# Kernel tuning notes

Measured on AMD Instinct MI355X. Metric: run time of the kernel, lower is better.

## Reference

```python
import jax, jax.numpy as jnp
import numpy as np

DN = ('NCHW', 'OIHW', 'NCHW')

def conv(x, w, b=None, stride=(1, 1), pad=((0, 0), (0, 0))):
    y = jax.lax.conv_general_dilated(x, w, stride, pad, dimension_numbers=DN)
    return y if b is None else y + b[None, :, None, None]

def conv_t(x, w, b, stride, pad):
    # PyTorch ConvTranspose2d: weight (in, out, kH, kW), output (H-1)*s - 2p + k
    kH, kW = w.shape[2], w.shape[3]
    wt = jnp.flip(w, axis=(2, 3)).swapaxes(0, 1)  # -> (out, in, kH, kW)
    y = jax.lax.conv_general_dilated(
        x, wt, (1, 1),
        ((kH - 1 - pad[0], kH - 1 - pad[0]), (kW - 1 - pad[1], kW - 1 - pad[1])),
        lhs_dilation=stride, dimension_numbers=DN)
    return y + b[None, :, None, None]

def res_stack(x, rw1, rw2):
    # Residual: x + conv1x1(relu(conv3x3(relu(x)))), then final relu
    for i in range(rw1.shape[0]):
        h = conv(jax.nn.relu(x), rw1[i], None, (1, 1), ((1, 1), (1, 1)))
        h = conv(jax.nn.relu(h), rw2[i], None, (1, 1), ((0, 0), (0, 0)))
        x = x + h
    return jax.nn.relu(x)

def setup_inputs() -> dict:
    key = jax.random.key(0)
    ks = jax.random.split(key, 24)
    def w(i, shape, s=0.05):
        return jax.random.normal(ks[i], shape, jnp.float32) * s
    K, D = 512, 64
    inp = {
        'x': jax.random.normal(ks[0], (32, 2, 400, 600), jnp.float32),
        'enc_w1': w(1, (64, 2, 10, 11)), 'enc_b1': w(2, (64,)),
        'enc_w2': w(3, (128, 64, 12, 12), 0.02), 'enc_b2': w(4, (128,)),
        'enc_w3': w(5, (128, 128, 3, 3)), 'enc_b3': w(6, (128,)),
        'enc_res_w1': w(7, (2, 64, 128, 3, 3)), 'enc_res_w2': w(8, (2, 128, 64, 1, 1)),
        'pre_w': w(9, (64, 128, 1, 1)), 'pre_b': w(10, (64,)),
        'emb': jax.random.uniform(ks[11], (K, D), jnp.float32, -1.0 / K, 1.0 / K),
        'dec_w1': w(12, (128, 64, 3, 3)), 'dec_b1': w(13, (128,)),
        'dec_res_w1': w(14, (2, 64, 128, 3, 3)), 'dec_res_w2': w(15, (2, 128, 64, 1, 1)),
        'dec_tw1': w(16, (128, 64, 12, 12), 0.02), 'dec_tb1': w(17, (64,)),
        'dec_tw2': w(18, (64, 2, 10, 11)), 'dec_tb2': w(19, (2,)),
        'reset': 0,
    }
    return inp

def reference(x, enc_w1, enc_b1, enc_w2, enc_b2, enc_w3, enc_b3, enc_res_w1,
              enc_res_w2, pre_w, pre_b, emb, dec_w1, dec_b1, dec_res_w1,
              dec_res_w2, dec_tw1, dec_tb1, dec_tw2, dec_tb2, reset):
    commitment_cost = 0.25
    K = emb.shape[0]
    # Encoder
    h = jax.nn.relu(conv(x, enc_w1, enc_b1, (8, 9), ((1, 1), (1, 1))))
    h = jax.nn.relu(conv(h, enc_w2, enc_b2, (10, 10), ((1, 1), (1, 1))))
    h = conv(h, enc_w3, enc_b3, (1, 1), ((1, 1), (1, 1)))
    h = res_stack(h, enc_res_w1, enc_res_w2)
    z = conv(h, pre_w, pre_b)  # [B, D, H, W]
    # VectorQuantizer (eval mode)
    zin = z.transpose(0, 2, 3, 1)  # [B, H, W, D]
    B, H, W, D = zin.shape
    flat = zin.reshape(-1, D)
    dist = (jnp.sum(flat ** 2, axis=1, keepdims=True)
            + jnp.sum(emb ** 2, axis=1)
            - 2.0 * flat @ emb.T)  # [N, K]
    idx = jnp.argmin(dist, axis=1)  # [N]
    q = emb[idx].reshape(B, H, W, D)
    e_latent = jnp.mean((jax.lax.stop_gradient(q) - zin) ** 2)
    q_latent = jnp.mean((q - jax.lax.stop_gradient(zin)) ** 2)
    loss = q_latent + commitment_cost * e_latent
    q_st = zin + jax.lax.stop_gradient(q - zin)  # straight-through
    counts = jnp.zeros((K,), jnp.float32).at[idx].add(1.0)
    avg_probs = counts / flat.shape[0]
    perplexity = jnp.exp(-jnp.sum(avg_probs * jnp.log(avg_probs + 1e-10)))
    q_nchw = q_st.transpose(0, 3, 1, 2)
    # Decoder
    d = conv(q_nchw, dec_w1, dec_b1, (1, 1), ((1, 1), (1, 1)))
    d = res_stack(d, dec_res_w1, dec_res_w2)
    d = jax.nn.relu(conv_t(d, dec_tw1, dec_tb1, (10, 10), (1, 1)))
    recon = conv_t(d, dec_tw2, dec_tb2, (8, 9), (1, 1))
    return loss, recon, perplexity
```

## Files before the change

kernel.cpp:

```cpp
#include <hip/hip_runtime.h>
#include <math.h>


__global__ __launch_bounds__(256) void conv1_k(const float* __restrict__ x,
                                               const float* __restrict__ w,
                                               const float* __restrict__ b,
                                               float* __restrict__ y)
{
    __shared__ float xs[2 * 10 * 596];
    const int blk = blockIdx.x;
    const int n = blk / 50, oh = blk % 50;
    const int tid = threadIdx.x;
    const int ih0 = oh * 8 - 1;
    for (int i = tid; i < 2 * 10 * 596; i += 256) {
        int c = i / 5960, rem = i % 5960;
        int r = rem / 596, j = rem % 596;
        int ih = ih0 + r, iw = j - 1;
        float v = 0.f;
        if (ih >= 0 && ih < 400 && iw >= 0 && iw < 600)
            v = x[((n * 2 + c) * 400 + ih) * 600 + iw];
        xs[i] = v;
    }
    __syncthreads();
    for (int i = tid; i < 32 * 66; i += 256) {
        int oc = i / 66, ow = i % 66;
        int col = ow * 9;
        float a0 = 0.f, a1 = 0.f;
        for (int c = 0; c < 2; ++c) {
            const float* wp0 = w + ((oc)      * 2 + c) * 110;
            const float* wp1 = w + ((oc + 32) * 2 + c) * 110;
            const float* xp  = xs + c * 5960 + col;
            for (int kh = 0; kh < 10; ++kh) {
                #pragma unroll
                for (int kw = 0; kw < 11; ++kw) {
                    float xv = xp[kh * 596 + kw];
                    a0 += xv * wp0[kh * 11 + kw];
                    a1 += xv * wp1[kh * 11 + kw];
                }
            }
        }
        y[((n * 64 + oc)      * 50 + oh) * 66 + ow] = fmaxf(a0 + b[oc], 0.f);
        y[((n * 64 + oc + 32) * 50 + oh) * 66 + ow] = fmaxf(a1 + b[oc + 32], 0.f);
    }
}

__global__ __launch_bounds__(256) void repack_oihw_k(const float* __restrict__ w,
                                                     float* __restrict__ wt,
                                                     int OC, int IC, int KH, int KW)
{
    int i = blockIdx.x * 256 + threadIdx.x;
    int total = OC * IC * KH * KW;
    if (i >= total) return;
    int oc = i % OC; int t = i / OC;
    int kw = t % KW; int kh = (t / KW) % KH; int c = t / (KW * KH);
    wt[i] = w[((oc * IC + c) * KH + kh) * KW + kw];
}

__global__ __launch_bounds__(256) void repack_iohw_k(const float* __restrict__ w,
                                                     float* __restrict__ wt,
                                                     int IC, int OC, int KH, int KW)
{
    int i = blockIdx.x * 256 + threadIdx.x;
    int total = OC * IC * KH * KW;
    if (i >= total) return;
    int oc = i % OC; int t = i / OC;
    int kw = t % KW; int kh = (t / KW) % KH; int c = t / (KW * KH);
    wt[i] = w[((c * OC + oc) * KH + kh) * KW + kw];
}

__global__ __launch_bounds__(512) void conv2_k2(const float* __restrict__ x,
                                                const float* __restrict__ wt,
                                                const float* __restrict__ b,
                                                float* __restrict__ y)
{
    __shared__ float xs[16 * 12 * 64];
    __shared__ float sred[4 * 128 * 6];
    const int tid = threadIdx.x;
    const int oc = tid & 127, sub = tid >> 7;
    const int n = blockIdx.x / 5, oh = blockIdx.x % 5;
    const int ih0 = oh * 10 - 1;
    float acc[6] = {0, 0, 0, 0, 0, 0};
    for (int cc = 0; cc < 4; ++cc) {
        __syncthreads();
        for (int i = tid; i < 12288; i += 512) {
            int col = i & 63; int t2 = i >> 6;
            int r = t2 % 12; int c = t2 / 12;
            int ih = ih0 + r, iw = col - 1;
            float v = 0.f;
            if (ih >= 0 && ih < 50 && iw >= 0 && iw < 66)
                v = x[((n * 64 + cc * 16 + c) * 50 + ih) * 66 + iw];
            xs[i] = v;
        }
        __syncthreads();
        for (int c = 0; c < 16; ++c) {
            for (int kh = sub * 3; kh < sub * 3 + 3; ++kh) {
                float xr[64];
                #pragma unroll
                for (int k = 0; k < 16; ++k)
                    *(float4*)&xr[4 * k] = *(const float4*)&xs[(c * 12 + kh) * 64 + 4 * k];
                const float* wp = wt + ((cc * 16 + c) * 144 + kh * 12) * 128 + oc;
                #pragma unroll
                for (int kw = 0; kw < 12; ++kw) {
                    float wv = wp[kw * 128];
                    #pragma unroll
                    for (int ow = 0; ow < 6; ++ow)
                        acc[ow] += xr[ow * 10 + kw] * wv;
                }
            }
        }
    }
    for (int j = 0; j < 6; ++j) sred[(sub * 128 + oc) * 6 + j] = acc[j];
    __syncthreads();
    if (sub == 0) {
        float bias = b[oc];
        #pragma unroll
        for (int j = 0; j < 6; ++j) {
            float v = acc[j] + sred[(128 + oc) * 6 + j] + sred[(256 + oc) * 6 + j]
                    + sred[(384 + oc) * 6 + j] + bias;
            y[((n * 128 + oc) * 5 + oh) * 6 + j] = fmaxf(v, 0.f);
        }
    }
}

__global__ void conv3x3_k(const float* __restrict__ x, const float* __restrict__ w,
                          const float* __restrict__ b, float* __restrict__ y,
                          int Cin, int Cout, int relu_in)
{
    int idx = blockIdx.x * 256 + threadIdx.x;
    int total = 32 * Cout * 30;
    if (idx >= total) return;
    int ow = idx % 6, t = idx / 6;
    int oh = t % 5; t /= 5;
    int oc = t % Cout;
    int n = t / Cout;
    float acc = b ? b[oc] : 0.f;
    for (int kh = 0; kh < 3; ++kh) {
        int ih = oh - 1 + kh;
        if (ih < 0 || ih >= 5) continue;
        for (int kw = 0; kw < 3; ++kw) {
            int iw = ow - 1 + kw;
            if (iw < 0 || iw >= 6) continue;
            const float* xp = x + (n * Cin * 5 + ih) * 6 + iw;
            const float* wp = w + (oc * Cin * 3 + kh) * 3 + kw;
            #pragma unroll 4
            for (int c = 0; c < Cin; ++c) {
                float xv = xp[c * 30];
                if (relu_in) xv = fmaxf(xv, 0.f);
                acc += xv * wp[c * 9];
            }
        }
    }
    y[idx] = acc;
}

__global__ void res2_k(float* __restrict__ x, const float* __restrict__ t,
                       const float* __restrict__ w)
{
    int idx = blockIdx.x * 256 + threadIdx.x;
    if (idx >= 32 * 128 * 30) return;
    int ow = idx % 6;
    int oh = (idx / 6) % 5;
    int oc = (idx / 30) % 128;
    int n = idx / 3840;
    const float* tp = t + (n * 64 * 5 + oh) * 6 + ow;
    const float* wp = w + oc * 64;
    float acc = 0.f;
    #pragma unroll 4
    for (int c = 0; c < 64; ++c) acc += fmaxf(tp[c * 30], 0.f) * wp[c];
    x[idx] += acc;
}

__global__ void conv1x1_k(const float* __restrict__ x, const float* __restrict__ w,
                          const float* __restrict__ b, float* __restrict__ y)
{
    int idx = blockIdx.x * 256 + threadIdx.x;
    if (idx >= 32 * 64 * 30) return;
    int ow = idx % 6;
    int oh = (idx / 6) % 5;
    int oc = (idx / 30) % 64;
    int n = idx / 1920;
    const float* xp = x + (n * 128 * 5 + oh) * 6 + ow;
    const float* wp = w + oc * 128;
    float acc = b[oc];
    #pragma unroll 4
    for (int c = 0; c < 128; ++c) acc += fmaxf(xp[c * 30], 0.f) * wp[c];
    y[idx] = acc;
}

__global__ __launch_bounds__(64) void vq_k(const float* __restrict__ z,
                                           const float* __restrict__ emb,
                                           float* __restrict__ qn,
                                           float* __restrict__ counts,
                                           float* __restrict__ loss_sum)
{
    const int r = blockIdx.x;
    const int lane = threadIdx.x;
    const int n = r / 30, hw = r % 30;
    __shared__ float zs[64];
    zs[lane] = z[(n * 64 + lane) * 30 + hw];
    __syncthreads();
    float best = 1e30f;
    int bestk = 0;
    for (int j = 0; j < 8; ++j) {
        int k = lane + j * 64;
        const float* ep = emb + k * 64;
        float dist = 0.f;
        #pragma unroll 8
        for (int d = 0; d < 64; ++d) {
            float df = ep[d] - zs[d];
            dist += df * df;
        }
        if (dist < best) { best = dist; bestk = k; }
    }
    for (int off = 32; off > 0; off >>= 1) {
        float ob = __shfl_down(best, off);
        int ok = __shfl_down(bestk, off);
        if (ob < best || (ob == best && ok < bestk)) { best = ob; bestk = ok; }
    }
    bestk = __shfl(bestk, 0);
    float ev = emb[bestk * 64 + lane];
    qn[(n * 64 + lane) * 30 + hw] = ev;
    float df = ev - zs[lane];
    df *= df;
    for (int off = 32; off > 0; off >>= 1) df += __shfl_down(df, off);
    if (lane == 0) {
        atomicAdd(loss_sum, df);
        atomicAdd(&counts[bestk], 1.0f);
    }
}

__global__ __launch_bounds__(256) void xpad_k(const float* __restrict__ h,
                                              float* __restrict__ xp)
{
    int i = blockIdx.x * 256 + threadIdx.x;
    if (i >= 32 * 128 * 7 * 8) return;
    int col = i & 7; int t = i >> 3;
    int row = t % 7; t /= 7;
    int c = t % 128; int n = t / 128;
    float v = 0.f;
    if (row >= 1 && row <= 5 && col >= 1 && col <= 6)
        v = fmaxf(h[((n * 128 + c) * 5 + row - 1) * 6 + col - 1], 0.f);
    xp[i] = v;
}

__global__ __launch_bounds__(256) void convt1_k2(const float* __restrict__ xp,
                                                 const float* __restrict__ wt,
                                                 const float* __restrict__ b,
                                                 float* __restrict__ y)
{
    int gtid = blockIdx.x * 256 + threadIdx.x;
    int item = gtid >> 6;
    int lane = threadIdx.x & 63;
    int rw = item % 10; int t = item / 10;
    int rh = t % 10; t /= 10;
    int io = t % 5; int n = t / 5;
    int oh = 10 * io + (rh == 0 ? 9 : rh - 1);
    int kh0, i0, kh1 = 0, i1 = 0, nh = 1;
    if (rh == 0)      { kh0 = 0;  i0 = io + 1; kh1 = 10; i1 = io;     nh = 2; }
    else if (rh == 1) { kh0 = 1;  i0 = io;     kh1 = 11; i1 = io - 1; nh = 2; }
    else              { kh0 = rh; i0 = io; }
    int m0 = (rw == 0) ? 1 : 0;
    int kwa = rw, kwb = rw + 10;
    int nw = (rw < 2) ? 2 : 1;
    float acc[6] = {0, 0, 0, 0, 0, 0};
    for (int th = 0; th < nh; ++th) {
        int kh = th ? kh1 : kh0;
        int irow = th ? i1 : i0;
        const float* xr  = xp + ((n * 128) * 7 + irow + 1) * 8 + m0;
        const float* wpa = wt + (kh * 12 + kwa) * 64 + lane;
        const float* wpb = wt + (kh * 12 + kwb) * 64 + lane;
        for (int c = 0; c < 128; ++c) {
            float z[7];
            #pragma unroll
            for (int k = 0; k < 7; ++k) z[k] = xr[k];
            float wa = *wpa;
            #pragma unroll
            for (int j = 0; j < 6; ++j) acc[j] += z[j + 1] * wa;
            if (nw == 2) {
                float wb = *wpb;
                #pragma unroll
                for (int j = 0; j < 6; ++j) acc[j] += z[j] * wb;
            }
            xr += 56; wpa += 9216; wpb += 9216;
        }
    }
    float bias = b[lane];
    int colb = 10 * m0 + rw;
    float* yp = y + ((n * 64 + lane) * 52 + (oh + 1)) * 62 + colb;
    #pragma unroll
    for (int j = 0; j < 6; ++j) yp[10 * j] = fmaxf(acc[j] + bias, 0.f);
}

__global__ __launch_bounds__(256) void convt2_k2(const float* __restrict__ xd,
                                                 const float* __restrict__ wt2g,
                                                 const float* __restrict__ bb,
                                                 float* __restrict__ out)
{
    __shared__ __align__(16) float wl[14080];
    for (int i = threadIdx.x; i < 14080; i += 256) wl[i] = wt2g[i];
    __syncthreads();
    const int tid0 = blockIdx.x * 256 + threadIdx.x;
    const float b0 = bb[0], b1 = bb[1];
    for (int s = 0; s < 5; ++s) {
        int item = tid0 + s * 230400;
        int g = item % 10; int t = item / 10;
        int rw = t % 9; t /= 9;
        int rh = t % 8; t /= 8;
        int io = t % 50; int n = t / 50;
        int oh = 8 * io + (rh == 0 ? 7 : rh - 1);
        int kh0, i0, kh1 = 0, i1 = 0, nh = 1;
        if (rh == 0)      { kh0 = 0;  i0 = io + 1; kh1 = 8; i1 = io;     nh = 2; }
        else if (rh == 1) { kh0 = 1;  i0 = io;     kh1 = 9; i1 = io - 1; nh = 2; }
        else              { kh0 = rh; i0 = io; }
        int m0 = ((rw == 0) ? 1 : 0) + g * 6;
        int kwa = rw, kwb = rw + 9;
        int nw = (rw < 2) ? 2 : 1;
        float a0[6] = {0, 0, 0, 0, 0, 0}, a1[6] = {0, 0, 0, 0, 0, 0};
        for (int th = 0; th < nh; ++th) {
            int kh = th ? kh1 : kh0;
            int irow = th ? i1 : i0;
            const float* xr  = xd + ((n * 64) * 52 + irow + 1) * 62 + m0;
            const float* wpa = wl + (kh * 11 + kwa) * 2;
            const float* wpb = wl + (kh * 11 + kwb) * 2;
            for (int c = 0; c < 64; ++c) {
                float z[7];
                #pragma unroll
                for (int k = 0; k < 7; ++k) z[k] = xr[k];
                float2 wa = *(const float2*)wpa;
                #pragma unroll
                for (int j = 0; j < 6; ++j) { a0[j] += z[j + 1] * wa.x; a1[j] += z[j + 1] * wa.y; }
                if (nw == 2) {
                    float2 wb = *(const float2*)wpb;
                    #pragma unroll
                    for (int j = 0; j < 6; ++j) { a0[j] += z[j] * wb.x; a1[j] += z[j] * wb.y; }
                }
                xr += 3224; wpa += 220; wpb += 220;
            }
        }
        int colb = 9 * m0 + rw - 1;
        float* yp0 = out + ((n * 2 + 0) * 400 + oh) * 540 + colb;
        float* yp1 = out + ((n * 2 + 1) * 400 + oh) * 540 + colb;
        #pragma unroll
        for (int j = 0; j < 6; ++j) { yp0[9 * j] = a0[j] + b0; yp1[9 * j] = a1[j] + b1; }
    }
}

__global__ __launch_bounds__(512) void fin_k(const float* __restrict__ counts,
                                             const float* __restrict__ loss_sum,
                                             float* __restrict__ out, int out_size)
{
    __shared__ float red[512];
    int t = threadIdx.x;
    float c = counts[t];
    float p = c * (1.0f / 960.0f);
    red[t] = p * logf(p + 1e-10f);
    __syncthreads();
    for (int s = 256; s > 0; s >>= 1) {
        if (t < s) red[t] += red[t + s];
        __syncthreads();
    }
    if (t == 0) {
        out[out_size - 1] = expf(-red[0]);
        out[0] = loss_sum[0] * 1.25f / 61440.0f;
    }
}

extern "C" void kernel_launch(void* const* d_in, const int* in_sizes, int n_in,
                              void* d_out, int out_size, void* d_ws, size_t ws_size,
                              hipStream_t stream)
{
    const float* x          = (const float*)d_in[0];
    const float* enc_w1     = (const float*)d_in[1];
    const float* enc_b1     = (const float*)d_in[2];
    const float* enc_w2     = (const float*)d_in[3];
    const float* enc_b2     = (const float*)d_in[4];
    const float* enc_w3     = (const float*)d_in[5];
    const float* enc_b3     = (const float*)d_in[6];
    const float* enc_res_w1 = (const float*)d_in[7];
    const float* enc_res_w2 = (const float*)d_in[8];
    const float* pre_w      = (const float*)d_in[9];
    const float* pre_b      = (const float*)d_in[10];
    const float* emb        = (const float*)d_in[11];
    const float* dec_w1     = (const float*)d_in[12];
    const float* dec_b1     = (const float*)d_in[13];
    const float* dec_res_w1 = (const float*)d_in[14];
    const float* dec_res_w2 = (const float*)d_in[15];
    const float* dec_tw1    = (const float*)d_in[16];
    const float* dec_tb1    = (const float*)d_in[17];
    const float* dec_tw2    = (const float*)d_in[18];
    const float* dec_tb2    = (const float*)d_in[19];

    float* ws  = (float*)d_ws;
    float* out = (float*)d_out;

    float* h1       = ws;
    float* h2       = ws + 6758400;
    float* hA       = ws + 6881280;
    float* t64      = ws + 7004160;
    float* z        = ws + 7065600;
    float* qn       = ws + 7127040;
    float* counts   = ws + 7188480;
    float* loss_sum = ws + 7188992;
    float* wtA      = ws + 7189056;
    float* wt2      = ws + 8368704;
    float* xpad     = ws + 8382784;
    float* dmid     = ws;

    hipMemsetAsync(counts, 0, 513 * sizeof(float), stream);

    repack_oihw_k<<<4608, 256, 0, stream>>>(enc_w2, wtA, 128, 64, 12, 12);
    conv1_k<<<1600, 256, 0, stream>>>(x, enc_w1, enc_b1, h1);
    conv2_k2<<<160, 512, 0, stream>>>(h1, wtA, enc_b2, h2);
    conv3x3_k<<<480, 256, 0, stream>>>(h2, enc_w3, enc_b3, hA, 128, 128, 0);
    for (int i = 0; i < 2; ++i) {
        conv3x3_k<<<240, 256, 0, stream>>>(hA, enc_res_w1 + i * 73728, nullptr, t64, 128, 64, 1);
        res2_k<<<480, 256, 0, stream>>>(hA, t64, enc_res_w2 + i * 8192);
    }
    conv1x1_k<<<240, 256, 0, stream>>>(hA, pre_w, pre_b, z);

    repack_iohw_k<<<4608, 256, 0, stream>>>(dec_tw1, wtA, 128, 64, 12, 12);
    repack_iohw_k<<<55, 256, 0, stream>>>(dec_tw2, wt2, 64, 2, 10, 11);

    vq_k<<<960, 64, 0, stream>>>(z, emb, qn, counts, loss_sum);

    conv3x3_k<<<480, 256, 0, stream>>>(qn, dec_w1, dec_b1, h2, 64, 128, 0);
    for (int i = 0; i < 2; ++i) {
        conv3x3_k<<<240, 256, 0, stream>>>(h2, dec_res_w1 + i * 73728, nullptr, t64, 128, 64, 1);
        res2_k<<<480, 256, 0, stream>>>(h2, t64, dec_res_w2 + i * 8192);
    }
    xpad_k<<<896, 256, 0, stream>>>(h2, xpad);
    hipMemsetAsync(dmid, 0, (size_t)6601728 * sizeof(float), stream);
    convt1_k2<<<4000, 256, 0, stream>>>(xpad, wtA, dec_tb1, dmid);
    convt2_k2<<<900, 256, 0, stream>>>(dmid, wt2, dec_tb2, out + 1);

    fin_k<<<1, 512, 0, stream>>>(counts, loss_sum, out, out_size);
}
```

Baseline: 1.858 ms.

## Fuse latent-stage convs and VQ into one per-sample kernel; retile transposed convs

Replaces the chain of small latent-resolution kernels (enc conv3, residual stacks, pre-conv, VQ, decoder conv1, decoder residuals, padding) with a single 32-block kernel that keeps activations in LDS, using pre-repacked weights. Both transposed-conv kernels are rewritten so each block stages its input rows in LDS and reuses them across output phases. This removes many launches and global round-trips, but the fused kernel runs on only 32 blocks, which may leave most of the GPU idle.

```diff
diff --git a/kernel.cpp b/kernel.cpp
--- a/kernel.cpp
+++ b/kernel.cpp
@@ -66,6 +66,37 @@
     int oc = i % OC; int t = i / OC;
     int kw = t % KW; int kh = (t / KW) % KH; int c = t / (KW * KH);
     wt[i] = w[((c * OC + oc) * KH + kh) * KW + kw];
+}
+
+__device__ __forceinline__ float fetch_oihw(const float* __restrict__ w, int j,
+                                            int OC, int IC, int KH, int KW)
+{
+    int oc = j % OC; int t = j / OC;
+    int kw = t % KW; int kh = (t / KW) % KH; int c = t / (KW * KH);
+    return w[((oc * IC + c) * KH + kh) * KW + kw];
+}
+
+__global__ __launch_bounds__(256) void repack_small_k(
+    const float* __restrict__ enc_w3, const float* __restrict__ er1,
+    const float* __restrict__ er2, const float* __restrict__ pre_w,
+    const float* __restrict__ dec_w1, const float* __restrict__ dr1,
+    const float* __restrict__ dr2, float* __restrict__ dst)
+{
+    int i = blockIdx.x * 256 + threadIdx.x;
+    if (i >= 557056) return;
+    float v;
+    if (i < 147456)       v = fetch_oihw(enc_w3,        i,          128, 128, 3, 3);
+    else if (i < 221184)  v = fetch_oihw(er1,           i - 147456,  64, 128, 3, 3);
+    else if (i < 294912)  v = fetch_oihw(er1 + 73728,   i - 221184,  64, 128, 3, 3);
+    else if (i < 303104)  v = fetch_oihw(er2,           i - 294912, 128,  64, 1, 1);
+    else if (i < 311296)  v = fetch_oihw(er2 + 8192,    i - 303104, 128,  64, 1, 1);
+    else if (i < 319488)  v = fetch_oihw(pre_w,         i - 311296,  64, 128, 1, 1);
+    else if (i < 393216)  v = fetch_oihw(dec_w1,        i - 319488, 128,  64, 3, 3);
+    else if (i < 466944)  v = fetch_oihw(dr1,           i - 393216,  64, 128, 3, 3);
+    else if (i < 540672)  v = fetch_oihw(dr1 + 73728,   i - 466944,  64, 128, 3, 3);
+    else if (i < 548864)  v = fetch_oihw(dr2,           i - 540672, 128,  64, 1, 1);
+    else                  v = fetch_oihw(dr2 + 8192,    i - 548864, 128,  64, 1, 1);
+    dst[i] = v;
 }
 
 __global__ __launch_bounds__(512) void conv2_k2(const float* __restrict__ x,
@@ -122,226 +153,300 @@
     }
 }
 
-__global__ void conv3x3_k(const float* __restrict__ x, const float* __restrict__ w,
-                          const float* __restrict__ b, float* __restrict__ y,
-                          int Cin, int Cout, int relu_in)
-{
-    int idx = blockIdx.x * 256 + threadIdx.x;
-    int total = 32 * Cout * 30;
-    if (idx >= total) return;
-    int ow = idx % 6, t = idx / 6;
-    int oh = t % 5; t /= 5;
-    int oc = t % Cout;
-    int n = t / Cout;
-    float acc = b ? b[oc] : 0.f;
-    for (int kh = 0; kh < 3; ++kh) {
-        int ih = oh - 1 + kh;
-        if (ih < 0 || ih >= 5) continue;
-        for (int kw = 0; kw < 3; ++kw) {
-            int iw = ow - 1 + kw;
-            if (iw < 0 || iw >= 6) continue;
-            const float* xp = x + (n * Cin * 5 + ih) * 6 + iw;
-            const float* wp = w + (oc * Cin * 3 + kh) * 3 + kw;
-            #pragma unroll 4
-            for (int c = 0; c < Cin; ++c) {
-                float xv = xp[c * 30];
-                if (relu_in) xv = fmaxf(xv, 0.f);
-                acc += xv * wp[c * 9];
+
+template<int CIN, int COUT, bool RELU_IN>
+__device__ __forceinline__ void conv3x3_lds(const float* __restrict__ src,
+                                            const float* __restrict__ w,
+                                            const float* __restrict__ bias,
+                                            float* __restrict__ dst, int tid)
+{
+    constexpr int G = 512 / COUT;
+    const int oc = tid % COUT;
+    const int g  = tid / COUT;
+    const int px0 = (30 * g) / G;
+    const int np  = (30 * (g + 1)) / G - px0;
+    float bv = bias ? bias[oc] : 0.f;
+    float acc[8];
+    #pragma unroll
+    for (int j = 0; j < 8; ++j) acc[j] = bv;
+    for (int c = 0; c < CIN; ++c) {
+        const float* wc = w + c * 9 * COUT + oc;
+        const float* sc = src + c * 30;
+        #pragma unroll
+        for (int kh = 0; kh < 3; ++kh) {
+            #pragma unroll
+            for (int kw = 0; kw < 3; ++kw) {
+                float wv = wc[(kh * 3 + kw) * COUT];
+                #pragma unroll
+                for (int j = 0; j < 8; ++j) {
+                    if (j < np) {
+                        int px = px0 + j;
+                        int oh = px / 6, ow = px - oh * 6;
+                        int ih = oh + kh - 1, iw = ow + kw - 1;
+                        if ((unsigned)ih < 5u && (unsigned)iw < 6u) {
+                            float xv = sc[ih * 6 + iw];
+                            if (RELU_IN) xv = fmaxf(xv, 0.f);
+                            acc[j] += xv * wv;
+                        }
+                    }
+                }
             }
         }
     }
-    y[idx] = acc;
-}
-
-__global__ void res2_k(float* __restrict__ x, const float* __restrict__ t,
-                       const float* __restrict__ w)
-{
-    int idx = blockIdx.x * 256 + threadIdx.x;
-    if (idx >= 32 * 128 * 30) return;
-    int ow = idx % 6;
-    int oh = (idx / 6) % 5;
-    int oc = (idx / 30) % 128;
-    int n = idx / 3840;
-    const float* tp = t + (n * 64 * 5 + oh) * 6 + ow;
-    const float* wp = w + oc * 64;
-    float acc = 0.f;
-    #pragma unroll 4
-    for (int c = 0; c < 64; ++c) acc += fmaxf(tp[c * 30], 0.f) * wp[c];
-    x[idx] += acc;
-}
-
-__global__ void conv1x1_k(const float* __restrict__ x, const float* __restrict__ w,
-                          const float* __restrict__ b, float* __restrict__ y)
-{
-    int idx = blockIdx.x * 256 + threadIdx.x;
-    if (idx >= 32 * 64 * 30) return;
-    int ow = idx % 6;
-    int oh = (idx / 6) % 5;
-    int oc = (idx / 30) % 64;
-    int n = idx / 1920;
-    const float* xp = x + (n * 128 * 5 + oh) * 6 + ow;
-    const float* wp = w + oc * 128;
-    float acc = b[oc];
-    #pragma unroll 4
-    for (int c = 0; c < 128; ++c) acc += fmaxf(xp[c * 30], 0.f) * wp[c];
-    y[idx] = acc;
-}
-
-__global__ __launch_bounds__(64) void vq_k(const float* __restrict__ z,
-                                           const float* __restrict__ emb,
-                                           float* __restrict__ qn,
-                                           float* __restrict__ counts,
-                                           float* __restrict__ loss_sum)
-{
-    const int r = blockIdx.x;
-    const int lane = threadIdx.x;
-    const int n = r / 30, hw = r % 30;
-    __shared__ float zs[64];
-    zs[lane] = z[(n * 64 + lane) * 30 + hw];
-    __syncthreads();
-    float best = 1e30f;
-    int bestk = 0;
+    #pragma unroll
+    for (int j = 0; j < 8; ++j)
+        if (j < np) dst[oc * 30 + px0 + j] = acc[j];
+}
+
+template<int CIN, int COUT, bool RELU_IN, bool ACCUM>
+__device__ __forceinline__ void conv1x1_lds(const float* __restrict__ src,
+                                            const float* __restrict__ w,
+                                            const float* __restrict__ bias,
+                                            float* __restrict__ dst, int tid)
+{
+    constexpr int G = 512 / COUT;
+    const int oc = tid % COUT;
+    const int g  = tid / COUT;
+    const int px0 = (30 * g) / G;
+    const int np  = (30 * (g + 1)) / G - px0;
+    float bv = bias ? bias[oc] : 0.f;
+    float acc[8];
+    #pragma unroll
+    for (int j = 0; j < 8; ++j) acc[j] = bv;
+    for (int c = 0; c < CIN; ++c) {
+        float wv = w[c * COUT + oc];
+        #pragma unroll
+        for (int j = 0; j < 8; ++j) {
+            if (j < np) {
+                float xv = src[c * 30 + px0 + j];
+                if (RELU_IN) xv = fmaxf(xv, 0.f);
+                acc[j] += xv * wv;
+            }
+        }
+    }
+    #pragma unroll
     for (int j = 0; j < 8; ++j) {
-        int k = lane + j * 64;
-        const float* ep = emb + k * 64;
-        float dist = 0.f;
-        #pragma unroll 8
-        for (int d = 0; d < 64; ++d) {
-            float df = ep[d] - zs[d];
-            dist += df * df;
-        }
-        if (dist < best) { best = dist; bestk = k; }
-    }
-    for (int off = 32; off > 0; off >>= 1) {
-        float ob = __shfl_down(best, off);
-        int ok = __shfl_down(bestk, off);
-        if (ob < best || (ob == best && ok < bestk)) { best = ob; bestk = ok; }
-    }
-    bestk = __shfl(bestk, 0);
-    float ev = emb[bestk * 64 + lane];
-    qn[(n * 64 + lane) * 30 + hw] = ev;
-    float df = ev - zs[lane];
-    df *= df;
-    for (int off = 32; off > 0; off >>= 1) df += __shfl_down(df, off);
-    if (lane == 0) {
-        atomicAdd(loss_sum, df);
-        atomicAdd(&counts[bestk], 1.0f);
-    }
-}
-
-__global__ __launch_bounds__(256) void xpad_k(const float* __restrict__ h,
-                                              float* __restrict__ xp)
-{
-    int i = blockIdx.x * 256 + threadIdx.x;
-    if (i >= 32 * 128 * 7 * 8) return;
-    int col = i & 7; int t = i >> 3;
-    int row = t % 7; t /= 7;
-    int c = t % 128; int n = t / 128;
-    float v = 0.f;
-    if (row >= 1 && row <= 5 && col >= 1 && col <= 6)
-        v = fmaxf(h[((n * 128 + c) * 5 + row - 1) * 6 + col - 1], 0.f);
-    xp[i] = v;
-}
-
-__global__ __launch_bounds__(256) void convt1_k2(const float* __restrict__ xp,
+        if (j < np) {
+            if (ACCUM) dst[oc * 30 + px0 + j] += acc[j];
+            else       dst[oc * 30 + px0 + j] = acc[j];
+        }
+    }
+}
+
+__global__ __launch_bounds__(512) void chain_k(
+    const float* __restrict__ h2, const float* __restrict__ wsm,
+    const float* __restrict__ enc_b3, const float* __restrict__ pre_b,
+    const float* __restrict__ emb, const float* __restrict__ dec_b1,
+    float* __restrict__ xpad, float* __restrict__ counts,
+    float* __restrict__ loss_sum)
+{
+    __shared__ float A[3840], B[3840], T[1920], Z[1920];
+    const int n = blockIdx.x;
+    const int tid = threadIdx.x;
+    for (int i = tid; i < 3840; i += 512) A[i] = h2[n * 3840 + i];
+    __syncthreads();
+    conv3x3_lds<128, 128, false>(A, wsm, enc_b3, B, tid);
+    __syncthreads();
+    conv3x3_lds<128, 64, true>(B, wsm + 147456, nullptr, T, tid);
+    __syncthreads();
+    conv1x1_lds<64, 128, true, true>(T, wsm + 294912, nullptr, B, tid);
+    __syncthreads();
+    conv3x3_lds<128, 64, true>(B, wsm + 221184, nullptr, T, tid);
+    __syncthreads();
+    conv1x1_lds<64, 128, true, true>(T, wsm + 303104, nullptr, B, tid);
+    __syncthreads();
+    conv1x1_lds<128, 64, true, false>(B, wsm + 311296, pre_b, Z, tid);
+    __syncthreads();
+    const int lane = tid & 63, wid = tid >> 6;
+    for (int px = wid; px < 30; px += 8) {
+        float zr[64];
+        #pragma unroll
+        for (int d = 0; d < 64; ++d) zr[d] = Z[d * 30 + px];
+        float best = 1e30f; int bestk = 0;
+        for (int jk = 0; jk < 8; ++jk) {
+            int k = lane + jk * 64;
+            const float* ep = emb + k * 64;
+            float dist = 0.f;
+            #pragma unroll 8
+            for (int d = 0; d < 64; ++d) { float df = ep[d] - zr[d]; dist += df * df; }
+            if (dist < best) { best = dist; bestk = k; }
+        }
+        for (int off = 32; off; off >>= 1) {
+            float ob = __shfl_down(best, off); int ok = __shfl_down(bestk, off);
+            if (ob < best || (ob == best && ok < bestk)) { best = ob; bestk = ok; }
+        }
+        bestk = __shfl(bestk, 0);
+        float ev = emb[bestk * 64 + lane];
+        T[lane * 30 + px] = ev;
+        float df = ev - Z[lane * 30 + px]; df *= df;
+        for (int off = 32; off; off >>= 1) df += __shfl_down(df, off);
+        if (lane == 0) { atomicAdd(loss_sum, df); atomicAdd(&counts[bestk], 1.f); }
+    }
+    __syncthreads();
+    conv3x3_lds<64, 128, false>(T, wsm + 319488, dec_b1, A, tid);
+    __syncthreads();
+    conv3x3_lds<128, 64, true>(A, wsm + 393216, nullptr, T, tid);
+    __syncthreads();
+    conv1x1_lds<64, 128, true, true>(T, wsm + 540672, nullptr, A, tid);
+    __syncthreads();
+    conv3x3_lds<128, 64, true>(A, wsm + 466944, nullptr, T, tid);
+    __syncthreads();
+    conv1x1_lds<64, 128, true, true>(T, wsm + 548864, nullptr, A, tid);
+    __syncthreads();
+    for (int i = tid; i < 7168; i += 512) {
+        int col = i & 7, r = (i >> 3) % 7, c = i / 56;
+        float v = 0.f;
+        if (r >= 1 && r <= 5 && col >= 1 && col <= 6)
+            v = fmaxf(A[c * 30 + (r - 1) * 6 + col - 1], 0.f);
+        xpad[n * 7168 + i] = v;
+    }
+}
+
+
+template<bool TR, bool TS>
+__device__ __forceinline__ void ct1_accum(const float* __restrict__ xs0,
+                                          const float* __restrict__ xs1,
+                                          const float* __restrict__ wt,
+                                          int R, int S, int m0, int lane,
+                                          float acc[6])
+{
+    #pragma unroll 2
+    for (int c = 0; c < 128; ++c) {
+        float x1[7], x0[7];
+        #pragma unroll
+        for (int k = 0; k < 7; ++k) x1[k] = xs1[c * 8 + m0 + k];
+        if (TR) {
+            #pragma unroll
+            for (int k = 0; k < 7; ++k) x0[k] = xs0[c * 8 + m0 + k];
+        }
+        float wA = wt[(c * 144 + R * 12 + S) * 64 + lane];
+        #pragma unroll
+        for (int j = 0; j < 6; ++j) acc[j] += x1[j + 1] * wA;
+        if (TS) {
+            float wB = wt[(c * 144 + R * 12 + S + 10) * 64 + lane];
+            #pragma unroll
+            for (int j = 0; j < 6; ++j) acc[j] += x1[j] * wB;
+        }
+        if (TR) {
+            float wC = wt[(c * 144 + (R + 10) * 12 + S) * 64 + lane];
+            #pragma unroll
+            for (int j = 0; j < 6; ++j) acc[j] += x0[j + 1] * wC;
+            if (TS) {
+                float wD = wt[(c * 144 + (R + 10) * 12 + S + 10) * 64 + lane];
+                #pragma unroll
+                for (int j = 0; j < 6; ++j) acc[j] += x0[j] * wD;
+            }
+        }
+    }
+}
+
+__global__ __launch_bounds__(256) void convt1_k3(const float* __restrict__ xp,
                                                  const float* __restrict__ wt,
                                                  const float* __restrict__ b,
                                                  float* __restrict__ y)
 {
-    int gtid = blockIdx.x * 256 + threadIdx.x;
-    int item = gtid >> 6;
-    int lane = threadIdx.x & 63;
-    int rw = item % 10; int t = item / 10;
-    int rh = t % 10; t /= 10;
-    int io = t % 5; int n = t / 5;
-    int oh = 10 * io + (rh == 0 ? 9 : rh - 1);
-    int kh0, i0, kh1 = 0, i1 = 0, nh = 1;
-    if (rh == 0)      { kh0 = 0;  i0 = io + 1; kh1 = 10; i1 = io;     nh = 2; }
-    else if (rh == 1) { kh0 = 1;  i0 = io;     kh1 = 11; i1 = io - 1; nh = 2; }
-    else              { kh0 = rh; i0 = io; }
-    int m0 = (rw == 0) ? 1 : 0;
-    int kwa = rw, kwb = rw + 10;
-    int nw = (rw < 2) ? 2 : 1;
-    float acc[6] = {0, 0, 0, 0, 0, 0};
-    for (int th = 0; th < nh; ++th) {
-        int kh = th ? kh1 : kh0;
-        int irow = th ? i1 : i0;
-        const float* xr  = xp + ((n * 128) * 7 + irow + 1) * 8 + m0;
-        const float* wpa = wt + (kh * 12 + kwa) * 64 + lane;
-        const float* wpb = wt + (kh * 12 + kwb) * 64 + lane;
-        for (int c = 0; c < 128; ++c) {
-            float z[7];
-            #pragma unroll
-            for (int k = 0; k < 7; ++k) z[k] = xr[k];
-            float wa = *wpa;
-            #pragma unroll
-            for (int j = 0; j < 6; ++j) acc[j] += z[j + 1] * wa;
-            if (nw == 2) {
-                float wb = *wpb;
-                #pragma unroll
-                for (int j = 0; j < 6; ++j) acc[j] += z[j] * wb;
+    __shared__ float xs[2][128][8];
+    const int bi = blockIdx.x;
+    const int n = bi / 50, oh = bi % 50;
+    const int q = (oh + 1) / 10, R = (oh + 1) % 10;
+    const int tid = threadIdx.x;
+    for (int i = tid; i < 2048; i += 256) {
+        int col = i & 7, c = (i >> 3) & 127, r = i >> 10;
+        ((float*)xs)[i] = xp[((n * 128 + c) * 7 + q + r) * 8 + col];
+    }
+    __syncthreads();
+    const int lane = tid & 63, wv = tid >> 6;
+    const float bias = b[lane];
+    const float* xs0 = &xs[0][0][0];
+    const float* xs1 = &xs[1][0][0];
+    for (int si = 0; si < 3; ++si) {
+        int S = wv + si * 4;
+        if (S >= 10) break;
+        int m0 = (S == 0) ? 1 : 0;
+        float acc[6] = {0, 0, 0, 0, 0, 0};
+        if (R < 2) {
+            if (S < 2) ct1_accum<true, true>(xs0, xs1, wt, R, S, m0, lane, acc);
+            else       ct1_accum<true, false>(xs0, xs1, wt, R, S, m0, lane, acc);
+        } else {
+            if (S < 2) ct1_accum<false, true>(xs0, xs1, wt, R, S, m0, lane, acc);
+            else       ct1_accum<false, false>(xs0, xs1, wt, R, S, m0, lane, acc);
+        }
+        float* yp = y + ((n * 64 + lane) * 52 + oh + 1) * 62 + 10 * m0 + S;
+        #pragma unroll
+        for (int j = 0; j < 6; ++j) yp[10 * j] = fmaxf(acc[j] + bias, 0.f);
+    }
+}
+
+
+template<bool TR, bool TS>
+__device__ __forceinline__ void ct2_accum(const float* __restrict__ xs0,
+                                          const float* __restrict__ xs1,
+                                          const float* __restrict__ wt2,
+                                          int R, int S, int m,
+                                          float& a0, float& a1)
+{
+    #pragma unroll 4
+    for (int c = 0; c < 64; ++c) {
+        float x1a = xs1[c * 64 + m + 1];
+        float2 wA = *(const float2*)&wt2[(c * 110 + R * 11 + S) * 2];
+        a0 += x1a * wA.x; a1 += x1a * wA.y;
+        if (TS) {
+            float x1b = xs1[c * 64 + m];
+            float2 wB = *(const float2*)&wt2[(c * 110 + R * 11 + S + 9) * 2];
+            a0 += x1b * wB.x; a1 += x1b * wB.y;
+        }
+        if (TR) {
+            float x0a = xs0[c * 64 + m + 1];
+            float2 wC = *(const float2*)&wt2[(c * 110 + (R + 8) * 11 + S) * 2];
+            a0 += x0a * wC.x; a1 += x0a * wC.y;
+            if (TS) {
+                float x0b = xs0[c * 64 + m];
+                float2 wD = *(const float2*)&wt2[(c * 110 + (R + 8) * 11 + S + 9) * 2];
+                a0 += x0b * wD.x; a1 += x0b * wD.y;
             }
-            xr += 56; wpa += 9216; wpb += 9216;
-        }
-    }
-    float bias = b[lane];
-    int colb = 10 * m0 + rw;
-    float* yp = y + ((n * 64 + lane) * 52 + (oh + 1)) * 62 + colb;
-    #pragma unroll
-    for (int j = 0; j < 6; ++j) yp[10 * j] = fmaxf(acc[j] + bias, 0.f);
-}
-
-__global__ __launch_bounds__(256) void convt2_k2(const float* __restrict__ xd,
-                                                 const float* __restrict__ wt2g,
+        }
+    }
+}
+
+__global__ __launch_bounds__(256) void convt2_k3(const float* __restrict__ xd,
+                                                 const float* __restrict__ wt2,
                                                  const float* __restrict__ bb,
                                                  float* __restrict__ out)
 {
-    __shared__ __align__(16) float wl[14080];
-    for (int i = threadIdx.x; i < 14080; i += 256) wl[i] = wt2g[i];
-    __syncthreads();
-    const int tid0 = blockIdx.x * 256 + threadIdx.x;
+    __shared__ float xs[2][64][64];
+    const int bi = blockIdx.x;
+    const int n = bi / 51, io = bi % 51;
+    const int tid = threadIdx.x;
+    for (int i = tid; i < 2 * 64 * 64; i += 256) {
+        int col = i & 63, c = (i >> 6) & 63, r = i >> 12;
+        float v = 0.f;
+        if (col < 62) v = xd[((n * 64 + c) * 52 + io + r) * 62 + col];
+        ((float*)xs)[i] = v;
+    }
+    __syncthreads();
     const float b0 = bb[0], b1 = bb[1];
-    for (int s = 0; s < 5; ++s) {
-        int item = tid0 + s * 230400;
-        int g = item % 10; int t = item / 10;
-        int rw = t % 9; t /= 9;
-        int rh = t % 8; t /= 8;
-        int io = t % 50; int n = t / 50;
-        int oh = 8 * io + (rh == 0 ? 7 : rh - 1);
-        int kh0, i0, kh1 = 0, i1 = 0, nh = 1;
-        if (rh == 0)      { kh0 = 0;  i0 = io + 1; kh1 = 8; i1 = io;     nh = 2; }
-        else if (rh == 1) { kh0 = 1;  i0 = io;     kh1 = 9; i1 = io - 1; nh = 2; }
-        else              { kh0 = rh; i0 = io; }
-        int m0 = ((rw == 0) ? 1 : 0) + g * 6;
-        int kwa = rw, kwb = rw + 9;
-        int nw = (rw < 2) ? 2 : 1;
-        float a0[6] = {0, 0, 0, 0, 0, 0}, a1[6] = {0, 0, 0, 0, 0, 0};
-        for (int th = 0; th < nh; ++th) {
-            int kh = th ? kh1 : kh0;
-            int irow = th ? i1 : i0;
-            const float* xr  = xd + ((n * 64) * 52 + irow + 1) * 62 + m0;
-            const float* wpa = wl + (kh * 11 + kwa) * 2;
-            const float* wpb = wl + (kh * 11 + kwb) * 2;
-            for (int c = 0; c < 64; ++c) {
-                float z[7];
-                #pragma unroll
-                for (int k = 0; k < 7; ++k) z[k] = xr[k];
-                float2 wa = *(const float2*)wpa;
-                #pragma unroll
-                for (int j = 0; j < 6; ++j) { a0[j] += z[j + 1] * wa.x; a1[j] += z[j + 1] * wa.y; }
-                if (nw == 2) {
-                    float2 wb = *(const float2*)wpb;
-                    #pragma unroll
-                    for (int j = 0; j < 6; ++j) { a0[j] += z[j] * wb.x; a1[j] += z[j] * wb.y; }
-                }
-                xr += 3224; wpa += 220; wpb += 220;
-            }
-        }
-        int colb = 9 * m0 + rw - 1;
-        float* yp0 = out + ((n * 2 + 0) * 400 + oh) * 540 + colb;
-        float* yp1 = out + ((n * 2 + 1) * 400 + oh) * 540 + colb;
-        #pragma unroll
-        for (int j = 0; j < 6; ++j) { yp0[9 * j] = a0[j] + b0; yp1[9 * j] = a1[j] + b1; }
+    const int lane = tid & 63, wv = tid >> 6;
+    if (lane >= 60) return;
+    const float* xs0 = &xs[0][0][0];
+    const float* xs1 = &xs[1][0][0];
+    for (int pp = 0; pp < 18; ++pp) {
+        int p = wv * 18 + pp;
+        int R = p / 9, S = p % 9;
+        int oh = 8 * io + R - 1;
+        if (oh < 0 || oh >= 400) continue;
+        int m = lane + ((S == 0) ? 1 : 0);
+        float a0 = 0.f, a1 = 0.f;
+        if (R < 2) {
+            if (S < 2) ct2_accum<true, true>(xs0, xs1, wt2, R, S, m, a0, a1);
+            else       ct2_accum<true, false>(xs0, xs1, wt2, R, S, m, a0, a1);
+        } else {
+            if (S < 2) ct2_accum<false, true>(xs0, xs1, wt2, R, S, m, a0, a1);
+            else       ct2_accum<false, false>(xs0, xs1, wt2, R, S, m, a0, a1);
+        }
+        int ow = 9 * m + S - 1;
+        float* yp = out + ((size_t)(n * 2) * 400 + oh) * 540 + ow;
+        yp[0] = a0 + b0;
+        yp[400 * 540] = a1 + b1;
     }
 }
 
@@ -394,44 +499,31 @@
     float* out = (float*)d_out;
 
     float* h1       = ws;
+    float* dmid     = ws;
     float* h2       = ws + 6758400;
-    float* hA       = ws + 6881280;
-    float* t64      = ws + 7004160;
-    float* z        = ws + 7065600;
-    float* qn       = ws + 7127040;
-    float* counts   = ws + 7188480;
-    float* loss_sum = ws + 7188992;
-    float* wtA      = ws + 7189056;
-    float* wt2      = ws + 8368704;
-    float* xpad     = ws + 8382784;
-    float* dmid     = ws;
+    float* counts   = ws + 6881280;
+    float* loss_sum = ws + 6881792;
+    float* wtA      = ws + 6881856;
+    float* wt2      = ws + 8061504;
+    float* xpad     = ws + 8075584;
+    float* wsm      = ws + 8304960;
 
     hipMemsetAsync(counts, 0, 513 * sizeof(float), stream);
 
     repack_oihw_k<<<4608, 256, 0, stream>>>(enc_w2, wtA, 128, 64, 12, 12);
     conv1_k<<<1600, 256, 0, stream>>>(x, enc_w1, enc_b1, h1);
     conv2_k2<<<160, 512, 0, stream>>>(h1, wtA, enc_b2, h2);
-    conv3x3_k<<<480, 256, 0, stream>>>(h2, enc_w3, enc_b3, hA, 128, 128, 0);
-    for (int i = 0; i < 2; ++i) {
-        conv3x3_k<<<240, 256, 0, stream>>>(hA, enc_res_w1 + i * 73728, nullptr, t64, 128, 64, 1);
-        res2_k<<<480, 256, 0, stream>>>(hA, t64, enc_res_w2 + i * 8192);
-    }
-    conv1x1_k<<<240, 256, 0, stream>>>(hA, pre_w, pre_b, z);
+
+    repack_small_k<<<2176, 256, 0, stream>>>(enc_w3, enc_res_w1, enc_res_w2, pre_w,
+                                             dec_w1, dec_res_w1, dec_res_w2, wsm);
+    chain_k<<<32, 512, 0, stream>>>(h2, wsm, enc_b3, pre_b, emb, dec_b1,
+                                    xpad, counts, loss_sum);
 
     repack_iohw_k<<<4608, 256, 0, stream>>>(dec_tw1, wtA, 128, 64, 12, 12);
     repack_iohw_k<<<55, 256, 0, stream>>>(dec_tw2, wt2, 64, 2, 10, 11);
-
-    vq_k<<<960, 64, 0, stream>>>(z, emb, qn, counts, loss_sum);
-
-    conv3x3_k<<<480, 256, 0, stream>>>(qn, dec_w1, dec_b1, h2, 64, 128, 0);
-    for (int i = 0; i < 2; ++i) {
-        conv3x3_k<<<240, 256, 0, stream>>>(h2, dec_res_w1 + i * 73728, nullptr, t64, 128, 64, 1);
-        res2_k<<<480, 256, 0, stream>>>(h2, t64, dec_res_w2 + i * 8192);
-    }
-    xpad_k<<<896, 256, 0, stream>>>(h2, xpad);
-    hipMemsetAsync(dmid, 0, (size_t)6601728 * sizeof(float), stream);
-    convt1_k2<<<4000, 256, 0, stream>>>(xpad, wtA, dec_tb1, dmid);
-    convt2_k2<<<900, 256, 0, stream>>>(dmid, wt2, dec_tb2, out + 1);
+    hipMemsetAsync(dmid, 0, (size_t)6602752 * sizeof(float), stream);
+    convt1_k3<<<1600, 256, 0, stream>>>(xpad, wtA, dec_tb1, dmid);
+    convt2_k3<<<1632, 256, 0, stream>>>(dmid, wt2, dec_tb2, out + 1);
 
     fin_k<<<1, 512, 0, stream>>>(counts, loss_sum, out, out_size);
 }
```

Result: slower. 3.949 ms (+112.5%).
